# Optimization experiments

Measured on AMD Instinct MI355X. Metric: run time of the kernel, lower is better.

Reference implementation:

```python
import jax, jax.numpy as jnp
import numpy as np

E = 16        # n_routed_experts
K = 4         # num_experts_per_tok
G = 4         # n_group
TG = 2        # topk_group
NS = 2        # n_shared_experts
H = 1024      # hidden_size
I = 1408      # intermediate_size
SCALE = 1.0   # routed_scaling_factor


def _gate(x2d, gate_w, gate_bias):
    # x2d: [T,H], gate_w: [E,H], gate_bias: [E]
    T = x2d.shape[0]
    logits = x2d.astype(jnp.float32) @ gate_w.astype(jnp.float32).T   # [T,E]
    scores = jax.nn.sigmoid(logits)
    sfc = scores + gate_bias[None, :]
    # group scores = sum of top-2 expert scores within each group
    grp = sfc.reshape(T, G, E // G)
    top2, _ = jax.lax.top_k(grp, 2)
    group_scores = top2.sum(-1)                                       # [T,G]
    _, gidx = jax.lax.top_k(group_scores, TG)                         # [T,TG]
    gmask = jnp.zeros((T, G), sfc.dtype).at[jnp.arange(T)[:, None], gidx].set(1.0)
    smask = jnp.repeat(gmask, E // G, axis=1) > 0                     # [T,E]
    tmp = jnp.where(smask, sfc, 0.0)
    _, topk_idx = jax.lax.top_k(tmp, K)                               # [T,K]
    topk_w = jnp.take_along_axis(scores, topk_idx, axis=1)            # [T,K]
    topk_w = topk_w / (topk_w.sum(-1, keepdims=True) + 1e-20)         # norm_topk_prob
    return topk_idx, topk_w * SCALE


def setup_inputs() -> dict:
    key = jax.random.key(0)
    ks = jax.random.split(key, 8)
    bound = 1.0 / np.sqrt(H)  # kaiming_uniform(a=sqrt(5)) on [E,H]
    return {
        "hidden_states": jax.random.normal(ks[0], (1, 1024, H), jnp.float32),
        "gate_w": jax.random.uniform(ks[1], (E, H), jnp.float32, -bound, bound),
        "gate_bias": jnp.zeros((E,), jnp.float32),
        "gate_proj": jax.random.normal(ks[2], (E, I, H), jnp.float32) * 0.02,
        "up_proj": jax.random.normal(ks[3], (E, I, H), jnp.float32) * 0.02,
        "down_proj": jax.random.normal(ks[4], (E, H, I), jnp.float32) * 0.02,
        "shared_gate_w": jax.random.normal(ks[5], (I * NS, H), jnp.float32) * 0.02,
        "shared_up_w": jax.random.normal(ks[6], (I * NS, H), jnp.float32) * 0.02,
        "shared_down_w": jax.random.normal(ks[7], (H, I * NS), jnp.float32) * 0.02,
    }


def reference(hidden_states, gate_w, gate_bias, gate_proj, up_proj, down_proj,
              shared_gate_w, shared_up_w, shared_down_w):
    orig_shape = hidden_states.shape
    x = hidden_states.reshape(-1, H)                                  # [T,H]
    topk_idx, topk_w = _gate(x, gate_w, gate_bias)
    # per-token per-expert combine weight (top-k indices are unique per token,
    # so scatter-add combine == dense weighted sum)
    combine_w = (jax.nn.one_hot(topk_idx, E, dtype=x.dtype) * topk_w[..., None]).sum(1)  # [T,E]
    g = jnp.einsum('th,eih->tei', x, gate_proj)                       # [T,E,I]
    u = jnp.einsum('th,eih->tei', x, up_proj)
    act = jax.nn.silu(g) * u                                          # SwiGLU
    y = jnp.einsum('tei,ehi,te->th', act, down_proj, combine_w)       # [T,H]
    # shared experts
    sg = x @ shared_gate_w.T
    su = x @ shared_up_w.T
    y = y + (jax.nn.silu(sg) * su) @ shared_down_w.T
    return y.reshape(orig_shape)
```

## Files before the change

### kernel.cpp

```cpp
#include <hip/hip_runtime.h>
#include <hip/hip_bf16.h>

#define T_TOK 1024
#define H_DIM 1024
#define I_DIM 1408
#define NE 16
#define NEP 18
#define BM 256
#define LDB 40

typedef __attribute__((ext_vector_type(8))) __bf16 bf16x8;
typedef __attribute__((ext_vector_type(4))) float f32x4;

__device__ __forceinline__ bf16x8 cvt8(float4 a, float4 b) {
    bf16x8 r;
    r[0] = (__bf16)a.x; r[1] = (__bf16)a.y; r[2] = (__bf16)a.z; r[3] = (__bf16)a.w;
    r[4] = (__bf16)b.x; r[5] = (__bf16)b.y; r[6] = (__bf16)b.z; r[7] = (__bf16)b.w;
    return r;
}

__global__ __launch_bounds__(64) void gate_kernel(
    const float* __restrict__ x, const float* __restrict__ gw,
    const float* __restrict__ gb,
    int* __restrict__ counts, int* __restrict__ etok, float* __restrict__ ew)
{
    const int t = blockIdx.x;
    const int lane = threadIdx.x;
    float s[NE];
#pragma unroll
    for (int e = 0; e < NE; ++e) s[e] = 0.f;
    const float* xr = x + (size_t)t * H_DIM;
    for (int i = lane; i < H_DIM; i += 64) {
        float xv = xr[i];
#pragma unroll
        for (int e = 0; e < NE; ++e) s[e] += xv * gw[e * H_DIM + i];
    }
#pragma unroll
    for (int e = 0; e < NE; ++e) {
        for (int off = 32; off > 0; off >>= 1) s[e] += __shfl_xor(s[e], off);
    }
    if (lane == 0) {
        float scores[NE], sfc[NE];
#pragma unroll
        for (int e = 0; e < NE; ++e) {
            scores[e] = 1.f / (1.f + __expf(-s[e]));
            sfc[e] = scores[e] + gb[e];
        }
        float gsc[4];
#pragma unroll
        for (int g = 0; g < 4; ++g) {
            float m1 = -1e30f, m2 = -1e30f;
#pragma unroll
            for (int j = 0; j < 4; ++j) {
                float v = sfc[4 * g + j];
                if (v > m1) { m2 = m1; m1 = v; } else if (v > m2) { m2 = v; }
            }
            gsc[g] = m1 + m2;
        }
        int g1 = 0;
        for (int g = 1; g < 4; ++g) if (gsc[g] > gsc[g1]) g1 = g;
        int g2 = -1;
        for (int g = 0; g < 4; ++g) {
            if (g == g1) continue;
            if (g2 < 0 || gsc[g] > gsc[g2]) g2 = g;
        }
        float tmp[NE];
#pragma unroll
        for (int e = 0; e < NE; ++e) {
            int gg = e >> 2;
            tmp[e] = (gg == g1 || gg == g2) ? sfc[e] : 0.0f;
        }
        int idxs[4]; float wk[4]; float wsum = 0.f;
#pragma unroll
        for (int k = 0; k < 4; ++k) {
            int bi = 0;
            for (int e = 1; e < NE; ++e) if (tmp[e] > tmp[bi]) bi = e;
            idxs[k] = bi; wk[k] = scores[bi]; wsum += scores[bi];
            tmp[bi] = -1e30f;
        }
        float inv = 1.f / (wsum + 1e-20f);
        for (int k = 0; k < 4; ++k) {
            int e = idxs[k];
            int pos = atomicAdd(&counts[e], 1);
            etok[e * T_TOK + pos] = t;
            ew[e * T_TOK + pos] = wk[k] * inv;
        }
    }
}

__global__ __launch_bounds__(256) void cvtx_kernel(
    const float* __restrict__ x, __hip_bfloat16* __restrict__ x_bf)
{
    int i = (blockIdx.x * 256 + threadIdx.x) * 4;
    float4 v = ((const float4*)x)[i >> 2];
    x_bf[i + 0] = __float2bfloat16(v.x);
    x_bf[i + 1] = __float2bfloat16(v.y);
    x_bf[i + 2] = __float2bfloat16(v.z);
    x_bf[i + 3] = __float2bfloat16(v.w);
}

__global__ __launch_bounds__(256, 2) void gateup_kernel(
    const __hip_bfloat16* __restrict__ x_bf,
    const float* __restrict__ gproj, const float* __restrict__ uproj,
    const float* __restrict__ sgw, const float* __restrict__ suw,
    const int* __restrict__ counts, const int* __restrict__ etok,
    __hip_bfloat16* __restrict__ act, int e0)
{
    const int slot = blockIdx.y;
    const int e = e0 + slot;
    const int cnt = (e < NE) ? counts[e] : T_TOK;
    const int row0 = blockIdx.z * BM;
    if (row0 >= cnt) return;

    __shared__ int toks[BM];
    __shared__ __hip_bfloat16 Bg[2][64 * LDB];
    __shared__ __hip_bfloat16 Bu[2][64 * LDB];

    const int tid = threadIdx.x;
    {
        int r = row0 + tid;
        toks[tid] = (e < NE) ? ((r < cnt) ? etok[e * T_TOK + r] : 0) : r;
    }

    const int nb0 = blockIdx.x * 64;
    const float *wg, *wu;
    if (e < NE) {
        wg = gproj + (size_t)e * I_DIM * H_DIM;
        wu = uproj + (size_t)e * I_DIM * H_DIM;
    } else {
        wg = sgw + (size_t)(e - NE) * I_DIM * H_DIM;
        wu = suw + (size_t)(e - NE) * I_DIM * H_DIM;
    }
    const int scol = tid >> 2, sq = tid & 3;
    const float* sgp = wg + (size_t)(nb0 + scol) * H_DIM + sq * 8;
    const float* sup = wu + (size_t)(nb0 + scol) * H_DIM + sq * 8;
    const int lws = scol * LDB + sq * 8;

    const int lane = tid & 63;
    const int w = tid >> 6;
    const int col = lane & 15, kq = lane >> 4;

    __syncthreads();

    const __hip_bfloat16* ar[4];
#pragma unroll
    for (int mi = 0; mi < 4; ++mi)
        ar[mi] = x_bf + (size_t)toks[w * 64 + mi * 16 + col] * H_DIM + kq * 8;

    f32x4 accg[4][4], accu[4][4];
#pragma unroll
    for (int mi = 0; mi < 4; ++mi)
#pragma unroll
        for (int ni = 0; ni < 4; ++ni) {
            accg[mi][ni] = (f32x4){0.f, 0.f, 0.f, 0.f};
            accu[mi][ni] = (f32x4){0.f, 0.f, 0.f, 0.f};
        }

    float4 ga = ((const float4*)sgp)[0], gb4 = ((const float4*)sgp)[1];
    float4 ua = ((const float4*)sup)[0], ub = ((const float4*)sup)[1];

    for (int k = 0; k < 32; ++k) {
        const int buf = k & 1;
        *(bf16x8*)&Bg[buf][lws] = cvt8(ga, gb4);
        *(bf16x8*)&Bu[buf][lws] = cvt8(ua, ub);
        __syncthreads();
        if (k < 31) {
            const float* pg = sgp + (k + 1) * 32;
            const float* pu = sup + (k + 1) * 32;
            ga = ((const float4*)pg)[0]; gb4 = ((const float4*)pg)[1];
            ua = ((const float4*)pu)[0]; ub = ((const float4*)pu)[1];
        }
        bf16x8 a[4], bg[4], bu[4];
#pragma unroll
        for (int mi = 0; mi < 4; ++mi) a[mi] = *(const bf16x8*)(ar[mi] + k * 32);
#pragma unroll
        for (int ni = 0; ni < 4; ++ni) {
            bg[ni] = *(const bf16x8*)&Bg[buf][(ni * 16 + col) * LDB + kq * 8];
            bu[ni] = *(const bf16x8*)&Bu[buf][(ni * 16 + col) * LDB + kq * 8];
        }
#pragma unroll
        for (int mi = 0; mi < 4; ++mi)
#pragma unroll
            for (int ni = 0; ni < 4; ++ni) {
                accg[mi][ni] = __builtin_amdgcn_mfma_f32_16x16x32_bf16(a[mi], bg[ni], accg[mi][ni], 0, 0, 0);
                accu[mi][ni] = __builtin_amdgcn_mfma_f32_16x16x32_bf16(a[mi], bu[ni], accu[mi][ni], 0, 0, 0);
            }
        __syncthreads();
    }

#pragma unroll
    for (int mi = 0; mi < 4; ++mi)
#pragma unroll
        for (int ni = 0; ni < 4; ++ni)
#pragma unroll
            for (int r = 0; r < 4; ++r) {
                int lrow = w * 64 + mi * 16 + kq * 4 + r;
                int grow = row0 + lrow;
                float g = accg[mi][ni][r];
                float a = (grow < cnt) ? (g / (1.f + __expf(-g)) * accu[mi][ni][r]) : 0.f;
                act[((size_t)slot * T_TOK + grow) * I_DIM + nb0 + ni * 16 + col] =
                    __float2bfloat16(a);
            }
}

__global__ __launch_bounds__(256, 2) void down_kernel(
    const __hip_bfloat16* __restrict__ act,
    const float* __restrict__ dproj, const float* __restrict__ sdw,
    const int* __restrict__ counts, const int* __restrict__ etok,
    const float* __restrict__ ew, float* __restrict__ y, int e0)
{
    const int slot = blockIdx.y;
    const int e = e0 + slot;
    const int cnt = (e < NE) ? counts[e] : T_TOK;
    const int row0 = blockIdx.z * BM;
    if (row0 >= cnt) return;

    __shared__ int toks[BM];
    __shared__ float wts[BM];
    __shared__ __hip_bfloat16 Bd[2][64 * LDB];

    const int tid = threadIdx.x;
    {
        int r = row0 + tid;
        if (e < NE) {
            bool ok = r < cnt;
            toks[tid] = ok ? etok[e * T_TOK + r] : 0;
            wts[tid]  = ok ? ew[e * T_TOK + r] : 0.f;
        } else { toks[tid] = r; wts[tid] = 1.f; }
    }

    const int nb0 = blockIdx.x * 64;
    const float* wd;
    int wstride;
    if (e < NE) { wd = dproj + (size_t)e * H_DIM * I_DIM; wstride = I_DIM; }
    else        { wd = sdw + (size_t)(e - NE) * I_DIM;    wstride = 2 * I_DIM; }
    const int scol = tid >> 2, sq = tid & 3;
    const float* sdp = wd + (size_t)(nb0 + scol) * wstride + sq * 8;
    const int lws = scol * LDB + sq * 8;

    const int lane = tid & 63;
    const int w = tid >> 6;
    const int col = lane & 15, kq = lane >> 4;

    __syncthreads();

    const __hip_bfloat16* ar[4];
#pragma unroll
    for (int mi = 0; mi < 4; ++mi)
        ar[mi] = act + ((size_t)slot * T_TOK + row0 + w * 64 + mi * 16 + col) * I_DIM + kq * 8;

    f32x4 acc[4][4];
#pragma unroll
    for (int mi = 0; mi < 4; ++mi)
#pragma unroll
        for (int ni = 0; ni < 4; ++ni) acc[mi][ni] = (f32x4){0.f, 0.f, 0.f, 0.f};

    float4 da = ((const float4*)sdp)[0], db = ((const float4*)sdp)[1];

    for (int k = 0; k < I_DIM / 32; ++k) {
        const int buf = k & 1;
        *(bf16x8*)&Bd[buf][lws] = cvt8(da, db);
        __syncthreads();
        if (k < I_DIM / 32 - 1) {
            const float* pd = sdp + (k + 1) * 32;
            da = ((const float4*)pd)[0]; db = ((const float4*)pd)[1];
        }
        bf16x8 a[4], b[4];
#pragma unroll
        for (int mi = 0; mi < 4; ++mi) a[mi] = *(const bf16x8*)(ar[mi] + k * 32);
#pragma unroll
        for (int ni = 0; ni < 4; ++ni)
            b[ni] = *(const bf16x8*)&Bd[buf][(ni * 16 + col) * LDB + kq * 8];
#pragma unroll
        for (int mi = 0; mi < 4; ++mi)
#pragma unroll
            for (int ni = 0; ni < 4; ++ni)
                acc[mi][ni] = __builtin_amdgcn_mfma_f32_16x16x32_bf16(a[mi], b[ni], acc[mi][ni], 0, 0, 0);
        __syncthreads();
    }

#pragma unroll
    for (int mi = 0; mi < 4; ++mi)
#pragma unroll
        for (int ni = 0; ni < 4; ++ni)
#pragma unroll
            for (int r = 0; r < 4; ++r) {
                int lrow = w * 64 + mi * 16 + kq * 4 + r;
                int grow = row0 + lrow;
                if (grow < cnt)
                    atomicAdd(&y[(size_t)toks[lrow] * H_DIM + nb0 + ni * 16 + col],
                              acc[mi][ni][r] * wts[lrow]);
            }
}

extern "C" void kernel_launch(void* const* d_in, const int* in_sizes, int n_in,
                              void* d_out, int out_size, void* d_ws, size_t ws_size,
                              hipStream_t stream) {
    (void)in_sizes; (void)n_in; (void)out_size;
    const float* x  = (const float*)d_in[0];
    const float* gw = (const float*)d_in[1];
    const float* gb = (const float*)d_in[2];
    const float* gp = (const float*)d_in[3];
    const float* up = (const float*)d_in[4];
    const float* dp = (const float*)d_in[5];
    const float* sg = (const float*)d_in[6];
    const float* su = (const float*)d_in[7];
    const float* sd = (const float*)d_in[8];
    float* out = (float*)d_out;

    char* ws = (char*)d_ws;
    int*   counts = (int*)ws;
    int*   etok   = (int*)(ws + 256);
    float* ew     = (float*)(ws + 256 + 65536);
    __hip_bfloat16* x_bf = (__hip_bfloat16*)(ws + 131328);
    __hip_bfloat16* act  = (__hip_bfloat16*)(ws + 2228480);

    size_t fixed = 2228480;
    size_t per_e = (size_t)T_TOK * I_DIM * 2;
    int cap = NEP;
    if (ws_size < fixed + (size_t)NEP * per_e) {
        cap = (ws_size > fixed + per_e) ? (int)((ws_size - fixed) / per_e) : 1;
        if (cap < 1) cap = 1;
    }

    hipMemsetAsync(ws, 0, 256, stream);
    hipMemsetAsync(out, 0, (size_t)T_TOK * H_DIM * 4, stream);

    gate_kernel<<<dim3(T_TOK), dim3(64), 0, stream>>>(x, gw, gb, counts, etok, ew);
    cvtx_kernel<<<dim3(1024), dim3(256), 0, stream>>>(x, x_bf);

    for (int e0 = 0; e0 < NEP; e0 += cap) {
        int ne = NEP - e0 < cap ? NEP - e0 : cap;
        gateup_kernel<<<dim3(I_DIM / 64, ne, T_TOK / BM), dim3(256), 0, stream>>>(
            x_bf, gp, up, sg, su, counts, etok, act, e0);
        down_kernel<<<dim3(H_DIM / 64, ne, T_TOK / BM), dim3(256), 0, stream>>>(
            act, dp, sd, counts, etok, ew, out, e0);
    }
}
```

Baseline: 536.6 us.

## Drop LDS staging for weights, use per-wave tiles, add atomic-free combine path

The gate-up and down GEMM kernels no longer stage fp32 weights through shared memory with block-wide barriers. Each lane now loads its own weight fragments straight into registers, and each wave exits independently when its 64-row slice is beyond the expert's token count. When the workspace is large enough, the down kernel writes per-expert outputs to a dense buffer, and a new combine kernel sums the four routed slots plus the two shared-expert slots per token. This replaces the atomicAdd scatter and the output memset. The cost is more redundant global and L2 weight traffic, since each wave reloads the weights, and a much larger workspace buffer.

Result: slower. 696.3 us (+29.7%).

```diff
diff --git a/kernel.cpp b/kernel.cpp
--- a/kernel.cpp
+++ b/kernel.cpp
@@ -7,7 +7,6 @@
 #define NE 16
 #define NEP 18
 #define BM 256
-#define LDB 40
 
 typedef __attribute__((ext_vector_type(8))) __bf16 bf16x8;
 typedef __attribute__((ext_vector_type(4))) float f32x4;
@@ -22,7 +21,8 @@
 __global__ __launch_bounds__(64) void gate_kernel(
     const float* __restrict__ x, const float* __restrict__ gw,
     const float* __restrict__ gb,
-    int* __restrict__ counts, int* __restrict__ etok, float* __restrict__ ew)
+    int* __restrict__ counts, int* __restrict__ etok, float* __restrict__ ew,
+    int* __restrict__ slotrow)
 {
     const int t = blockIdx.x;
     const int lane = threadIdx.x;
@@ -84,6 +84,7 @@
             int pos = atomicAdd(&counts[e], 1);
             etok[e * T_TOK + pos] = t;
             ew[e * T_TOK + pos] = wk[k] * inv;
+            slotrow[t * 4 + k] = e * T_TOK + pos;
         }
     }
 }
@@ -99,7 +100,7 @@
     x_bf[i + 3] = __float2bfloat16(v.w);
 }
 
-__global__ __launch_bounds__(256, 2) void gateup_kernel(
+__global__ __launch_bounds__(256) void gateup_kernel(
     const __hip_bfloat16* __restrict__ x_bf,
     const float* __restrict__ gproj, const float* __restrict__ uproj,
     const float* __restrict__ sgw, const float* __restrict__ suw,
@@ -109,20 +110,14 @@
     const int slot = blockIdx.y;
     const int e = e0 + slot;
     const int cnt = (e < NE) ? counts[e] : T_TOK;
-    const int row0 = blockIdx.z * BM;
-    if (row0 >= cnt) return;
-
-    __shared__ int toks[BM];
-    __shared__ __hip_bfloat16 Bg[2][64 * LDB];
-    __shared__ __hip_bfloat16 Bu[2][64 * LDB];
-
-    const int tid = threadIdx.x;
-    {
-        int r = row0 + tid;
-        toks[tid] = (e < NE) ? ((r < cnt) ? etok[e * T_TOK + r] : 0) : r;
-    }
-
+    const int w = threadIdx.x >> 6;
+    const int wrow0 = blockIdx.z * BM + w * 64;
+    if (wrow0 >= cnt) return;
+
+    const int lane = threadIdx.x & 63;
+    const int col = lane & 15, kq = lane >> 4;
     const int nb0 = blockIdx.x * 64;
+
     const float *wg, *wu;
     if (e < NE) {
         wg = gproj + (size_t)e * I_DIM * H_DIM;
@@ -131,21 +126,21 @@
         wg = sgw + (size_t)(e - NE) * I_DIM * H_DIM;
         wu = suw + (size_t)(e - NE) * I_DIM * H_DIM;
     }
-    const int scol = tid >> 2, sq = tid & 3;
-    const float* sgp = wg + (size_t)(nb0 + scol) * H_DIM + sq * 8;
-    const float* sup = wu + (size_t)(nb0 + scol) * H_DIM + sq * 8;
-    const int lws = scol * LDB + sq * 8;
-
-    const int lane = tid & 63;
-    const int w = tid >> 6;
-    const int col = lane & 15, kq = lane >> 4;
-
-    __syncthreads();
-
-    const __hip_bfloat16* ar[4];
-#pragma unroll
-    for (int mi = 0; mi < 4; ++mi)
-        ar[mi] = x_bf + (size_t)toks[w * 64 + mi * 16 + col] * H_DIM + kq * 8;
+
+    const __hip_bfloat16* ap[4];
+#pragma unroll
+    for (int mi = 0; mi < 4; ++mi) {
+        int gr = wrow0 + mi * 16 + col;
+        int tok = (e < NE) ? ((gr < cnt) ? etok[e * T_TOK + gr] : 0) : gr;
+        ap[mi] = x_bf + (size_t)tok * H_DIM + kq * 8;
+    }
+    const float* bgp[4];
+    const float* bup[4];
+#pragma unroll
+    for (int ni = 0; ni < 4; ++ni) {
+        bgp[ni] = wg + (size_t)(nb0 + ni * 16 + col) * H_DIM + kq * 8;
+        bup[ni] = wu + (size_t)(nb0 + ni * 16 + col) * H_DIM + kq * 8;
+    }
 
     f32x4 accg[4][4], accu[4][4];
 #pragma unroll
@@ -156,28 +151,32 @@
             accu[mi][ni] = (f32x4){0.f, 0.f, 0.f, 0.f};
         }
 
-    float4 ga = ((const float4*)sgp)[0], gb4 = ((const float4*)sgp)[1];
-    float4 ua = ((const float4*)sup)[0], ub = ((const float4*)sup)[1];
-
-    for (int k = 0; k < 32; ++k) {
-        const int buf = k & 1;
-        *(bf16x8*)&Bg[buf][lws] = cvt8(ga, gb4);
-        *(bf16x8*)&Bu[buf][lws] = cvt8(ua, ub);
-        __syncthreads();
-        if (k < 31) {
-            const float* pg = sgp + (k + 1) * 32;
-            const float* pu = sup + (k + 1) * 32;
-            ga = ((const float4*)pg)[0]; gb4 = ((const float4*)pg)[1];
-            ua = ((const float4*)pu)[0]; ub = ((const float4*)pu)[1];
-        }
-        bf16x8 a[4], bg[4], bu[4];
-#pragma unroll
-        for (int mi = 0; mi < 4; ++mi) a[mi] = *(const bf16x8*)(ar[mi] + k * 32);
+    float4 gs[4][2], us[4][2];
+#pragma unroll
+    for (int ni = 0; ni < 4; ++ni) {
+        gs[ni][0] = ((const float4*)bgp[ni])[0]; gs[ni][1] = ((const float4*)bgp[ni])[1];
+        us[ni][0] = ((const float4*)bup[ni])[0]; us[ni][1] = ((const float4*)bup[ni])[1];
+    }
+
+    for (int k = 0; k < H_DIM / 32; ++k) {
+        bf16x8 bg[4], bu[4];
 #pragma unroll
         for (int ni = 0; ni < 4; ++ni) {
-            bg[ni] = *(const bf16x8*)&Bg[buf][(ni * 16 + col) * LDB + kq * 8];
-            bu[ni] = *(const bf16x8*)&Bu[buf][(ni * 16 + col) * LDB + kq * 8];
-        }
+            bg[ni] = cvt8(gs[ni][0], gs[ni][1]);
+            bu[ni] = cvt8(us[ni][0], us[ni][1]);
+        }
+        if (k < H_DIM / 32 - 1) {
+#pragma unroll
+            for (int ni = 0; ni < 4; ++ni) {
+                const float4* pg = (const float4*)(bgp[ni] + (k + 1) * 32);
+                const float4* pu = (const float4*)(bup[ni] + (k + 1) * 32);
+                gs[ni][0] = pg[0]; gs[ni][1] = pg[1];
+                us[ni][0] = pu[0]; us[ni][1] = pu[1];
+            }
+        }
+        bf16x8 a[4];
+#pragma unroll
+        for (int mi = 0; mi < 4; ++mi) a[mi] = *(const bf16x8*)(ap[mi] + k * 32);
 #pragma unroll
         for (int mi = 0; mi < 4; ++mi)
 #pragma unroll
@@ -185,25 +184,26 @@
                 accg[mi][ni] = __builtin_amdgcn_mfma_f32_16x16x32_bf16(a[mi], bg[ni], accg[mi][ni], 0, 0, 0);
                 accu[mi][ni] = __builtin_amdgcn_mfma_f32_16x16x32_bf16(a[mi], bu[ni], accu[mi][ni], 0, 0, 0);
             }
-        __syncthreads();
-    }
-
-#pragma unroll
-    for (int mi = 0; mi < 4; ++mi)
-#pragma unroll
-        for (int ni = 0; ni < 4; ++ni)
-#pragma unroll
-            for (int r = 0; r < 4; ++r) {
-                int lrow = w * 64 + mi * 16 + kq * 4 + r;
-                int grow = row0 + lrow;
+    }
+
+#pragma unroll
+    for (int mi = 0; mi < 4; ++mi)
+#pragma unroll
+        for (int r = 0; r < 4; ++r) {
+            int grow = wrow0 + mi * 16 + kq * 4 + r;
+            bool live = grow < cnt;
+#pragma unroll
+            for (int ni = 0; ni < 4; ++ni) {
                 float g = accg[mi][ni][r];
-                float a = (grow < cnt) ? (g / (1.f + __expf(-g)) * accu[mi][ni][r]) : 0.f;
+                float a = live ? (g / (1.f + __expf(-g)) * accu[mi][ni][r]) : 0.f;
                 act[((size_t)slot * T_TOK + grow) * I_DIM + nb0 + ni * 16 + col] =
                     __float2bfloat16(a);
             }
-}
-
-__global__ __launch_bounds__(256, 2) void down_kernel(
+        }
+}
+
+template<bool COMBINE>
+__global__ __launch_bounds__(256) void down_kernel(
     const __hip_bfloat16* __restrict__ act,
     const float* __restrict__ dproj, const float* __restrict__ sdw,
     const int* __restrict__ counts, const int* __restrict__ etok,
@@ -212,42 +212,27 @@
     const int slot = blockIdx.y;
     const int e = e0 + slot;
     const int cnt = (e < NE) ? counts[e] : T_TOK;
-    const int row0 = blockIdx.z * BM;
-    if (row0 >= cnt) return;
-
-    __shared__ int toks[BM];
-    __shared__ float wts[BM];
-    __shared__ __hip_bfloat16 Bd[2][64 * LDB];
-
-    const int tid = threadIdx.x;
-    {
-        int r = row0 + tid;
-        if (e < NE) {
-            bool ok = r < cnt;
-            toks[tid] = ok ? etok[e * T_TOK + r] : 0;
-            wts[tid]  = ok ? ew[e * T_TOK + r] : 0.f;
-        } else { toks[tid] = r; wts[tid] = 1.f; }
-    }
-
+    const int w = threadIdx.x >> 6;
+    const int wrow0 = blockIdx.z * BM + w * 64;
+    if (wrow0 >= cnt) return;
+
+    const int lane = threadIdx.x & 63;
+    const int col = lane & 15, kq = lane >> 4;
     const int nb0 = blockIdx.x * 64;
+
     const float* wd;
     int wstride;
     if (e < NE) { wd = dproj + (size_t)e * H_DIM * I_DIM; wstride = I_DIM; }
     else        { wd = sdw + (size_t)(e - NE) * I_DIM;    wstride = 2 * I_DIM; }
-    const int scol = tid >> 2, sq = tid & 3;
-    const float* sdp = wd + (size_t)(nb0 + scol) * wstride + sq * 8;
-    const int lws = scol * LDB + sq * 8;
-
-    const int lane = tid & 63;
-    const int w = tid >> 6;
-    const int col = lane & 15, kq = lane >> 4;
-
-    __syncthreads();
-
-    const __hip_bfloat16* ar[4];
-#pragma unroll
-    for (int mi = 0; mi < 4; ++mi)
-        ar[mi] = act + ((size_t)slot * T_TOK + row0 + w * 64 + mi * 16 + col) * I_DIM + kq * 8;
+
+    const __hip_bfloat16* ap[4];
+#pragma unroll
+    for (int mi = 0; mi < 4; ++mi)
+        ap[mi] = act + ((size_t)slot * T_TOK + wrow0 + mi * 16 + col) * I_DIM + kq * 8;
+    const float* bdp[4];
+#pragma unroll
+    for (int ni = 0; ni < 4; ++ni)
+        bdp[ni] = wd + (size_t)(nb0 + ni * 16 + col) * wstride + kq * 8;
 
     f32x4 acc[4][4];
 #pragma unroll
@@ -255,42 +240,74 @@
 #pragma unroll
         for (int ni = 0; ni < 4; ++ni) acc[mi][ni] = (f32x4){0.f, 0.f, 0.f, 0.f};
 
-    float4 da = ((const float4*)sdp)[0], db = ((const float4*)sdp)[1];
+    float4 ds[4][2];
+#pragma unroll
+    for (int ni = 0; ni < 4; ++ni) {
+        ds[ni][0] = ((const float4*)bdp[ni])[0]; ds[ni][1] = ((const float4*)bdp[ni])[1];
+    }
 
     for (int k = 0; k < I_DIM / 32; ++k) {
-        const int buf = k & 1;
-        *(bf16x8*)&Bd[buf][lws] = cvt8(da, db);
-        __syncthreads();
+        bf16x8 bd[4];
+#pragma unroll
+        for (int ni = 0; ni < 4; ++ni) bd[ni] = cvt8(ds[ni][0], ds[ni][1]);
         if (k < I_DIM / 32 - 1) {
-            const float* pd = sdp + (k + 1) * 32;
-            da = ((const float4*)pd)[0]; db = ((const float4*)pd)[1];
-        }
-        bf16x8 a[4], b[4];
-#pragma unroll
-        for (int mi = 0; mi < 4; ++mi) a[mi] = *(const bf16x8*)(ar[mi] + k * 32);
-#pragma unroll
-        for (int ni = 0; ni < 4; ++ni)
-            b[ni] = *(const bf16x8*)&Bd[buf][(ni * 16 + col) * LDB + kq * 8];
+#pragma unroll
+            for (int ni = 0; ni < 4; ++ni) {
+                const float4* pd = (const float4*)(bdp[ni] + (k + 1) * 32);
+                ds[ni][0] = pd[0]; ds[ni][1] = pd[1];
+            }
+        }
+        bf16x8 a[4];
+#pragma unroll
+        for (int mi = 0; mi < 4; ++mi) a[mi] = *(const bf16x8*)(ap[mi] + k * 32);
 #pragma unroll
         for (int mi = 0; mi < 4; ++mi)
 #pragma unroll
             for (int ni = 0; ni < 4; ++ni)
-                acc[mi][ni] = __builtin_amdgcn_mfma_f32_16x16x32_bf16(a[mi], b[ni], acc[mi][ni], 0, 0, 0);
-        __syncthreads();
-    }
-
-#pragma unroll
-    for (int mi = 0; mi < 4; ++mi)
-#pragma unroll
-        for (int ni = 0; ni < 4; ++ni)
-#pragma unroll
-            for (int r = 0; r < 4; ++r) {
-                int lrow = w * 64 + mi * 16 + kq * 4 + r;
-                int grow = row0 + lrow;
-                if (grow < cnt)
-                    atomicAdd(&y[(size_t)toks[lrow] * H_DIM + nb0 + ni * 16 + col],
-                              acc[mi][ni][r] * wts[lrow]);
-            }
+                acc[mi][ni] = __builtin_amdgcn_mfma_f32_16x16x32_bf16(a[mi], bd[ni], acc[mi][ni], 0, 0, 0);
+    }
+
+#pragma unroll
+    for (int mi = 0; mi < 4; ++mi)
+#pragma unroll
+        for (int r = 0; r < 4; ++r) {
+            int grow = wrow0 + mi * 16 + kq * 4 + r;
+            if (grow >= cnt) continue;
+            if (COMBINE) {
+                float wt = (e < NE) ? ew[e * T_TOK + grow] : 1.f;
+#pragma unroll
+                for (int ni = 0; ni < 4; ++ni)
+                    y[((size_t)e * T_TOK + grow) * H_DIM + nb0 + ni * 16 + col] =
+                        acc[mi][ni][r] * wt;
+            } else {
+                float wt; int tokr;
+                if (e < NE) { wt = ew[e * T_TOK + grow]; tokr = etok[e * T_TOK + grow]; }
+                else        { wt = 1.f;                  tokr = grow; }
+#pragma unroll
+                for (int ni = 0; ni < 4; ++ni)
+                    atomicAdd(&y[(size_t)tokr * H_DIM + nb0 + ni * 16 + col],
+                              acc[mi][ni][r] * wt);
+            }
+        }
+}
+
+__global__ __launch_bounds__(256) void combine_kernel(
+    const float* __restrict__ dout, const int* __restrict__ slotrow,
+    float* __restrict__ out)
+{
+    const int t = blockIdx.x;
+    const int h4 = threadIdx.x;
+    const float4* d4 = (const float4*)dout;
+    float4 s0 = d4[((size_t)(16 * T_TOK + t)) * 256 + h4];
+    float4 s1 = d4[((size_t)(17 * T_TOK + t)) * 256 + h4];
+    float4 s = {s0.x + s1.x, s0.y + s1.y, s0.z + s1.z, s0.w + s1.w};
+#pragma unroll
+    for (int j = 0; j < 4; ++j) {
+        int sr = slotrow[t * 4 + j];
+        float4 v = d4[(size_t)sr * 256 + h4];
+        s.x += v.x; s.y += v.y; s.z += v.z; s.w += v.w;
+    }
+    ((float4*)out)[(size_t)t * 256 + h4] = s;
 }
 
 extern "C" void kernel_launch(void* const* d_in, const int* in_sizes, int n_in,
@@ -309,31 +326,42 @@
     float* out = (float*)d_out;
 
     char* ws = (char*)d_ws;
-    int*   counts = (int*)ws;
-    int*   etok   = (int*)(ws + 256);
-    float* ew     = (float*)(ws + 256 + 65536);
-    __hip_bfloat16* x_bf = (__hip_bfloat16*)(ws + 131328);
-    __hip_bfloat16* act  = (__hip_bfloat16*)(ws + 2228480);
-
-    size_t fixed = 2228480;
-    size_t per_e = (size_t)T_TOK * I_DIM * 2;
-    int cap = NEP;
-    if (ws_size < fixed + (size_t)NEP * per_e) {
-        cap = (ws_size > fixed + per_e) ? (int)((ws_size - fixed) / per_e) : 1;
-        if (cap < 1) cap = 1;
-    }
+    int*   counts  = (int*)ws;
+    int*   slotrow = (int*)(ws + 256);
+    int*   etok    = (int*)(ws + 16640);
+    float* ew      = (float*)(ws + 82176);
+    __hip_bfloat16* x_bf = (__hip_bfloat16*)(ws + 147712);
+    __hip_bfloat16* act  = (__hip_bfloat16*)(ws + 2244864);
+    float* dout    = (float*)(ws + 54149376);
+
+    const size_t need_combine = 54149376ull + (size_t)NEP * T_TOK * H_DIM * 4;
+    const bool combine = ws_size >= need_combine;
 
     hipMemsetAsync(ws, 0, 256, stream);
-    hipMemsetAsync(out, 0, (size_t)T_TOK * H_DIM * 4, stream);
-
-    gate_kernel<<<dim3(T_TOK), dim3(64), 0, stream>>>(x, gw, gb, counts, etok, ew);
+    gate_kernel<<<dim3(T_TOK), dim3(64), 0, stream>>>(x, gw, gb, counts, etok, ew, slotrow);
     cvtx_kernel<<<dim3(1024), dim3(256), 0, stream>>>(x, x_bf);
 
-    for (int e0 = 0; e0 < NEP; e0 += cap) {
-        int ne = NEP - e0 < cap ? NEP - e0 : cap;
-        gateup_kernel<<<dim3(I_DIM / 64, ne, T_TOK / BM), dim3(256), 0, stream>>>(
-            x_bf, gp, up, sg, su, counts, etok, act, e0);
-        down_kernel<<<dim3(H_DIM / 64, ne, T_TOK / BM), dim3(256), 0, stream>>>(
-            act, dp, sd, counts, etok, ew, out, e0);
-    }
-}
+    if (combine) {
+        gateup_kernel<<<dim3(I_DIM / 64, NEP, T_TOK / BM), dim3(256), 0, stream>>>(
+            x_bf, gp, up, sg, su, counts, etok, act, 0);
+        down_kernel<true><<<dim3(H_DIM / 64, NEP, T_TOK / BM), dim3(256), 0, stream>>>(
+            act, dp, sd, counts, etok, ew, dout, 0);
+        combine_kernel<<<dim3(T_TOK), dim3(256), 0, stream>>>(dout, slotrow, out);
+    } else {
+        size_t fixed = 2244864;
+        size_t per_e = (size_t)T_TOK * I_DIM * 2;
+        int cap = NEP;
+        if (ws_size < fixed + (size_t)NEP * per_e) {
+            cap = (ws_size > fixed + per_e) ? (int)((ws_size - fixed) / per_e) : 1;
+            if (cap < 1) cap = 1;
+        }
+        hipMemsetAsync(out, 0, (size_t)T_TOK * H_DIM * 4, stream);
+        for (int e0 = 0; e0 < NEP; e0 += cap) {
+            int ne = NEP - e0 < cap ? NEP - e0 : cap;
+            gateup_kernel<<<dim3(I_DIM / 64, ne, T_TOK / BM), dim3(256), 0, stream>>>(
+                x_bf, gp, up, sg, su, counts, etok, act, e0);
+            down_kernel<false><<<dim3(H_DIM / 64, ne, T_TOK / BM), dim3(256), 0, stream>>>(
+                act, dp, sd, counts, etok, ew, out, e0);
+        }
+    }
+}
```
